# Optimization experiments

Hardware: AMD Instinct MI355X
Metric: run time of the kernel (lower is better)

Reference implementation:

```python
import jax, jax.numpy as jnp
import numpy as np

N, E, IN_DIM, HID, HEADS, N_CLASSES, N_GRAPHS = 50000, 800000, 128, 64, 4, 16, 64
NEG_SLOPE = 0.2


def setup_inputs() -> dict:
    key = jax.random.key(0)
    ks = jax.random.split(key, 12)
    s = 0.1
    return {
        "x": jax.random.normal(ks[0], (N, IN_DIM), jnp.float32),
        "edge_index": jax.random.randint(ks[1], (2, E), 0, N, jnp.int32),
        "batch": jnp.sort(jax.random.randint(ks[2], (N,), 0, N_GRAPHS, jnp.int32)),
        "W1": jax.random.normal(ks[3], (IN_DIM, HEADS * HID), jnp.float32) * s,
        "a_src1": jax.random.normal(ks[4], (HEADS, HID), jnp.float32) * s,
        "a_dst1": jax.random.normal(ks[5], (HEADS, HID), jnp.float32) * s,
        "b1": jnp.zeros((HEADS * HID,), jnp.float32),
        "W2": jax.random.normal(ks[6], (HEADS * HID, HID), jnp.float32) * s,
        "a_src2": jax.random.normal(ks[7], (1, HID), jnp.float32) * s,
        "a_dst2": jax.random.normal(ks[8], (1, HID), jnp.float32) * s,
        "b2": jnp.zeros((HID,), jnp.float32),
        "fcW": jax.random.normal(ks[9], (HID, N_CLASSES), jnp.float32) * s,
        "fcb": jnp.zeros((N_CLASSES,), jnp.float32),
    }


def gat_conv(x, edge_index, W, a_src, a_dst, bias, concat):
    # PyG GATConv (eval mode): add self loops, per-head linear, additive attention,
    # segment softmax over incoming edges of each destination node, scatter-add.
    n = x.shape[0]
    heads, d = a_src.shape
    h = (x @ W).reshape(n, heads, d)                      # [n, H, d]
    asrc = jnp.einsum('nhd,hd->nh', h, a_src)             # [n, H]
    adst = jnp.einsum('nhd,hd->nh', h, a_dst)             # [n, H]
    loops = jnp.arange(n, dtype=edge_index.dtype)
    src = jnp.concatenate([edge_index[0], loops])         # message sources j
    dst = jnp.concatenate([edge_index[1], loops])         # targets i
    e = jax.nn.leaky_relu(asrc[src] + adst[dst], NEG_SLOPE)  # [E+n, H]
    m = jax.ops.segment_max(e, dst, num_segments=n)
    p = jnp.exp(e - m[dst])
    s = jax.ops.segment_sum(p, dst, num_segments=n)
    alpha = p / (s[dst] + 1e-16)                          # [E+n, H]
    msg = h[src] * alpha[:, :, None]                      # [E+n, H, d]
    out = jax.ops.segment_sum(msg, dst, num_segments=n)   # [n, H, d]
    out = out.reshape(n, heads * d) if concat else out.mean(axis=1)
    return out + bias


def reference(x, edge_index, batch, W1, a_src1, a_dst1, b1, W2, a_src2, a_dst2, b2, fcW, fcb):
    h = jax.nn.elu(gat_conv(x, edge_index, W1, a_src1, a_dst1, b1, True))
    h = gat_conv(h, edge_index, W2, a_src2, a_dst2, b2, False)
    # global_mean_pool over graph ids
    cnt = jax.ops.segment_sum(jnp.ones((h.shape[0],), h.dtype), batch, num_segments=N_GRAPHS)
    pooled = jax.ops.segment_sum(h, batch, num_segments=N_GRAPHS) / jnp.maximum(cnt, 1.0)[:, None]
    return pooled @ fcW + fcb
```

## Files before the change

kernel.cpp:

```cpp
#include <hip/hip_runtime.h>
#include <hip/hip_bf16.h>
#include <hip/hip_fp8.h>


#define Nn 50000
#define Ed 800000
#define NEG 0.2f
#define SCAN_B 196
#define EB 3125
#define GB 783

typedef __attribute__((ext_vector_type(8))) short short8;
typedef __attribute__((ext_vector_type(4))) float f32x4;
typedef __attribute__((ext_vector_type(2))) float f32x2;

#if defined(__has_builtin)
#if __has_builtin(__builtin_amdgcn_cvt_pk_f32_fp8) && __has_builtin(__builtin_amdgcn_cvt_pk_fp8_f32)
#define FP8_FAST 1
#endif
#endif
#ifndef FP8_FAST
#define FP8_FAST 0
#endif

__device__ __forceinline__ float lrelu(float x){ return fmaxf(x, NEG*x); }
__device__ __forceinline__ float bf2f(unsigned short u){ return __uint_as_float((unsigned)u << 16); }
__device__ __forceinline__ unsigned short f2bf(float f){
    __hip_bfloat16 b = __float2bfloat16(f);
    return *reinterpret_cast<unsigned short*>(&b);
}
__device__ __forceinline__ short f2bfs(float f){ return (short)f2bf(f); }

__device__ __forceinline__ unsigned char f2fp8(float f){
#if FP8_FAST
    int v = __builtin_amdgcn_cvt_pk_fp8_f32(f, f, 0, false);
    return (unsigned char)(v & 0xff);
#else
    __hip_fp8_e4m3 t(f);
    return (unsigned char)t.__x;
#endif
}

__device__ __forceinline__ float4 fp8x4_to_f32(unsigned int v){
#if FP8_FAST
    f32x2 lo = __builtin_amdgcn_cvt_pk_f32_fp8((int)v, false);
    f32x2 hi = __builtin_amdgcn_cvt_pk_f32_fp8((int)v, true);
    return make_float4(lo[0], lo[1], hi[0], hi[1]);
#else
    __hip_fp8_e4m3 t0, t1, t2, t3;
    t0.__x = (unsigned char)(v);
    t1.__x = (unsigned char)(v >> 8);
    t2.__x = (unsigned char)(v >> 16);
    t3.__x = (unsigned char)(v >> 24);
    return make_float4((float)t0, (float)t1, (float)t2, (float)t3);
#endif
}

__global__ void k_degree(const int* __restrict__ dst, int* __restrict__ deg,
                         const float* __restrict__ W1, const float* __restrict__ W2,
                         unsigned short* __restrict__ W1s, unsigned short* __restrict__ W2s){
    if (blockIdx.x < EB){
        int e = blockIdx.x*256 + threadIdx.x;
        if (e < Ed) atomicAdd(&deg[dst[e]], 1);
    } else {
        int t = (blockIdx.x - EB)*256 + threadIdx.x;
        if (t < 32768){
            int j = t & 7, lane = (t>>3) & 63, ks = (t>>9) & 3, nt = t>>11;
            int k = ks*32 + (lane>>4)*8 + j;
            int n = nt*16 + (lane&15);
            W1s[t] = f2bf(W1[k*256 + n]);
        }
        if (t < 16384){
            int j = t & 7, lane = (t>>3) & 63, ks = (t>>9) & 7, nt = t>>12;
            int k = ks*32 + (lane>>4)*8 + j;
            int n = nt*16 + (lane&15);
            W2s[t] = f2bf(W2[k*64 + n]);
        }
    }
}

__global__ __launch_bounds__(256) void k_partial(const int* __restrict__ deg, int* __restrict__ partial){
    __shared__ int red[256];
    int tid = threadIdx.x;
    int g = blockIdx.x*256 + tid;
    red[tid] = (g < Nn) ? deg[g] : 0;
    __syncthreads();
    for (int off = 128; off > 0; off >>= 1){
        if (tid < off) red[tid] += red[tid+off];
        __syncthreads();
    }
    if (tid == 0) partial[blockIdx.x] = red[0];
}

__global__ __launch_bounds__(256) void k_apply(const int* __restrict__ deg, const int* __restrict__ partial,
                                               int* __restrict__ rowptr, int* __restrict__ cursor){
    __shared__ int sp[256];
    __shared__ int s[256];
    __shared__ int blockoff;
    int tid = threadIdx.x;
    int pv = (tid < SCAN_B) ? partial[tid] : 0;
    sp[tid] = pv; __syncthreads();
    for (int off = 1; off < 256; off <<= 1){
        int t = (tid >= off) ? sp[tid-off] : 0;
        __syncthreads();
        sp[tid] += t;
        __syncthreads();
    }
    if (tid == (int)blockIdx.x) blockoff = sp[tid] - pv;
    if (blockIdx.x == 0 && tid == 255) rowptr[Nn] = sp[255];
    __syncthreads();
    int g = blockIdx.x*256 + tid;
    int v = (g < Nn) ? deg[g] : 0;
    s[tid] = v; __syncthreads();
    for (int off = 1; off < 256; off <<= 1){
        int t = (tid >= off) ? s[tid-off] : 0;
        __syncthreads();
        s[tid] += t;
        __syncthreads();
    }
    if (g < Nn){
        int ex = s[tid] - v + blockoff;
        rowptr[g] = ex;
        cursor[g] = ex;
    }
}

__global__ __launch_bounds__(256) void k_gemm1_scatter(
        const float* __restrict__ x, const unsigned short* __restrict__ W1s,
        const float* __restrict__ a_src, const float* __restrict__ a_dst,
        unsigned char* __restrict__ h1f8,
        float* __restrict__ asrc, float* __restrict__ adst,
        const int* __restrict__ esrc, const int* __restrict__ edst,
        int* __restrict__ cursor, int* __restrict__ csr){
    if (blockIdx.x >= GB){
        int e = (blockIdx.x - GB)*256 + threadIdx.x;
        if (e < Ed){
            int pos = atomicAdd(&cursor[edst[e]], 1);
            csr[pos] = esrc[e];
        }
        return;
    }
    int wv = blockIdx.x*4 + (threadIdx.x>>6);
    int lane = threadIdx.x & 63;
    int m0 = wv*16;
    if (m0 >= Nn) return;
    int quad = lane >> 4, col = lane & 15;
    int mrow = m0 + col;
    f32x4 acc[16] = {};
    const float* ap0 = &x[(size_t)mrow*128 + quad*8];
    #pragma unroll
    for (int ks = 0; ks < 4; ks++){
        float4 a0 = *(const float4*)(ap0 + ks*32);
        float4 a1 = *(const float4*)(ap0 + ks*32 + 4);
        short8 af;
        af[0]=f2bfs(a0.x); af[1]=f2bfs(a0.y); af[2]=f2bfs(a0.z); af[3]=f2bfs(a0.w);
        af[4]=f2bfs(a1.x); af[5]=f2bfs(a1.y); af[6]=f2bfs(a1.z); af[7]=f2bfs(a1.w);
        #pragma unroll
        for (int nt = 0; nt < 16; nt++){
            short8 bf = *(const short8*)&W1s[(size_t)(nt*4+ks)*512 + lane*8];
            acc[nt] = __builtin_amdgcn_mfma_f32_16x16x32_bf16(af, bf, acc[nt], 0, 0, 0);
        }
    }
    unsigned char* outp = &h1f8[(size_t)(m0 + quad*4)*256 + col];
    #pragma unroll
    for (int nt = 0; nt < 16; nt++)
        #pragma unroll
        for (int r = 0; r < 4; r++)
            outp[(size_t)r*256 + nt*16] = f2fp8(acc[nt][r]);
    float asf[16], adf[16];
    #pragma unroll
    for (int nt = 0; nt < 16; nt++){
        asf[nt] = a_src[nt*16 + col];
        adf[nt] = a_dst[nt*16 + col];
    }
    #pragma unroll
    for (int h = 0; h < 4; h++){
        #pragma unroll
        for (int r = 0; r < 4; r++){
            float ps = acc[4*h+0][r]*asf[4*h+0] + acc[4*h+1][r]*asf[4*h+1]
                     + acc[4*h+2][r]*asf[4*h+2] + acc[4*h+3][r]*asf[4*h+3];
            float pd = acc[4*h+0][r]*adf[4*h+0] + acc[4*h+1][r]*adf[4*h+1]
                     + acc[4*h+2][r]*adf[4*h+2] + acc[4*h+3][r]*adf[4*h+3];
            #pragma unroll
            for (int m = 1; m < 16; m <<= 1){ ps += __shfl_xor(ps, m); pd += __shfl_xor(pd, m); }
            if (col == h*4 + r){
                int n = m0 + quad*4 + r;
                asrc[n*4 + h] = ps;
                adst[n*4 + h] = pd;
            }
        }
    }
}

__global__ __launch_bounds__(256) void k_gemm2(const unsigned short* __restrict__ g1b,
                                               const unsigned short* __restrict__ W2s,
                                               const float* __restrict__ a_src, const float* __restrict__ a_dst,
                                               unsigned short* __restrict__ h2b,
                                               float* __restrict__ asrc, float* __restrict__ adst){
    int wv = blockIdx.x*4 + (threadIdx.x>>6);
    int lane = threadIdx.x & 63;
    int m0 = wv*16;
    if (m0 >= Nn) return;
    int quad = lane >> 4, col = lane & 15;
    int mrow = m0 + col;
    f32x4 acc[4] = {};
    const unsigned short* ap0 = &g1b[(size_t)mrow*256 + quad*8];
    #pragma unroll
    for (int ks = 0; ks < 8; ks++){
        short8 af = *(const short8*)(ap0 + ks*32);
        #pragma unroll
        for (int nt = 0; nt < 4; nt++){
            short8 bf = *(const short8*)&W2s[(size_t)(nt*8+ks)*512 + lane*8];
            acc[nt] = __builtin_amdgcn_mfma_f32_16x16x32_bf16(af, bf, acc[nt], 0, 0, 0);
        }
    }
    unsigned short* outp = &h2b[(size_t)(m0 + quad*4)*64 + col];
    #pragma unroll
    for (int nt = 0; nt < 4; nt++)
        #pragma unroll
        for (int r = 0; r < 4; r++)
            outp[(size_t)r*64 + nt*16] = f2bf(acc[nt][r]);
    float asf[4], adf[4];
    #pragma unroll
    for (int nt = 0; nt < 4; nt++){
        asf[nt] = a_src[nt*16 + col];
        adf[nt] = a_dst[nt*16 + col];
    }
    #pragma unroll
    for (int r = 0; r < 4; r++){
        float ps = acc[0][r]*asf[0] + acc[1][r]*asf[1] + acc[2][r]*asf[2] + acc[3][r]*asf[3];
        float pd = acc[0][r]*adf[0] + acc[1][r]*adf[1] + acc[2][r]*adf[2] + acc[3][r]*adf[3];
        #pragma unroll
        for (int m = 1; m < 16; m <<= 1){ ps += __shfl_xor(ps, m); pd += __shfl_xor(pd, m); }
        if (col == r){
            int n = m0 + quad*4 + r;
            asrc[n] = ps;
            adst[n] = pd;
        }
    }
}

__global__ __launch_bounds__(256) void k_aggr1(const unsigned char* __restrict__ h1f8,
                                               const float* __restrict__ asrc, const float* __restrict__ adst,
                                               const int* __restrict__ rowptr, const int* __restrict__ csr,
                                               const float* __restrict__ b1, unsigned short* __restrict__ g1){
    int w = threadIdx.x >> 6, lane = threadIdx.x & 63;
    int i = blockIdx.x*4 + w; if (i >= Nn) return;
    int hh = lane >> 4;
    float ad = adst[i*4 + hh];
    float as = asrc[i*4 + hh];
    float p = __expf(lrelu(as + ad));
    unsigned int hv = *(const unsigned int*)&h1f8[(size_t)i*256 + 4*lane];
    float4 hd = fp8x4_to_f32(hv);
    float acc0 = p*hd.x, acc1 = p*hd.y, acc2 = p*hd.z, acc3 = p*hd.w;
    float ssum = p;
    int beg = rowptr[i], end = rowptr[i+1];
    int j = beg;
    for (; j + 3 < end; j += 4){
        int s0 = csr[j], s1 = csr[j+1], s2 = csr[j+2], s3 = csr[j+3];
        float a0 = asrc[s0*4 + hh];
        float a1 = asrc[s1*4 + hh];
        float a2 = asrc[s2*4 + hh];
        float a3 = asrc[s3*4 + hh];
        unsigned int v0 = *(const unsigned int*)&h1f8[(size_t)s0*256 + 4*lane];
        unsigned int v1 = *(const unsigned int*)&h1f8[(size_t)s1*256 + 4*lane];
        unsigned int v2 = *(const unsigned int*)&h1f8[(size_t)s2*256 + 4*lane];
        unsigned int v3 = *(const unsigned int*)&h1f8[(size_t)s3*256 + 4*lane];
        float q0 = __expf(lrelu(a0 + ad));
        float q1 = __expf(lrelu(a1 + ad));
        float q2 = __expf(lrelu(a2 + ad));
        float q3 = __expf(lrelu(a3 + ad));
        float4 d0 = fp8x4_to_f32(v0);
        float4 d1 = fp8x4_to_f32(v1);
        float4 d2 = fp8x4_to_f32(v2);
        float4 d3 = fp8x4_to_f32(v3);
        acc0 += q0*d0.x + q1*d1.x + q2*d2.x + q3*d3.x;
        acc1 += q0*d0.y + q1*d1.y + q2*d2.y + q3*d3.y;
        acc2 += q0*d0.z + q1*d1.z + q2*d2.z + q3*d3.z;
        acc3 += q0*d0.w + q1*d1.w + q2*d2.w + q3*d3.w;
        ssum += q0 + q1 + q2 + q3;
    }
    for (; j < end; j++){
        int s = csr[j];
        float a = asrc[s*4 + hh];
        unsigned int v = *(const unsigned int*)&h1f8[(size_t)s*256 + 4*lane];
        float q = __expf(lrelu(a + ad));
        float4 d = fp8x4_to_f32(v);
        acc0 += q*d.x; acc1 += q*d.y; acc2 += q*d.z; acc3 += q*d.w;
        ssum += q;
    }
    float inv = 1.0f/(ssum + 1e-16f);
    float4 b4 = *(const float4*)&b1[4*lane];
    float o0 = acc0*inv + b4.x;
    float o1 = acc1*inv + b4.y;
    float o2 = acc2*inv + b4.z;
    float o3 = acc3*inv + b4.w;
    ushort4 o;
    o.x = f2bf(o0 > 0.f ? o0 : expm1f(o0));
    o.y = f2bf(o1 > 0.f ? o1 : expm1f(o1));
    o.z = f2bf(o2 > 0.f ? o2 : expm1f(o2));
    o.w = f2bf(o3 > 0.f ? o3 : expm1f(o3));
    *(ushort4*)&g1[(size_t)i*256 + 4*lane] = o;
}

__global__ __launch_bounds__(256) void k_aggr2(const unsigned short* __restrict__ h2,
                                               const float* __restrict__ asrc, const float* __restrict__ adst,
                                               const int* __restrict__ rowptr, const int* __restrict__ csr,
                                               unsigned short* __restrict__ g2){
    int w = threadIdx.x >> 6, lane = threadIdx.x & 63;
    int i = blockIdx.x*4 + w; if (i >= Nn) return;
    float ad = adst[i];
    float p = __expf(lrelu(asrc[i] + ad));
    float acc = p * bf2f(h2[(size_t)i*64 + lane]);
    float ss = p;
    int beg = rowptr[i], end = rowptr[i+1];
    int j = beg;
    for (; j + 3 < end; j += 4){
        int s0 = csr[j], s1 = csr[j+1], s2 = csr[j+2], s3 = csr[j+3];
        float a0 = asrc[s0], a1 = asrc[s1], a2 = asrc[s2], a3 = asrc[s3];
        unsigned short v0 = h2[(size_t)s0*64 + lane];
        unsigned short v1 = h2[(size_t)s1*64 + lane];
        unsigned short v2 = h2[(size_t)s2*64 + lane];
        unsigned short v3 = h2[(size_t)s3*64 + lane];
        float q0 = __expf(lrelu(a0 + ad));
        float q1 = __expf(lrelu(a1 + ad));
        float q2 = __expf(lrelu(a2 + ad));
        float q3 = __expf(lrelu(a3 + ad));
        acc += q0*bf2f(v0) + q1*bf2f(v1) + q2*bf2f(v2) + q3*bf2f(v3);
        ss += q0 + q1 + q2 + q3;
    }
    for (; j < end; j++){
        int s = csr[j];
        float q = __expf(lrelu(asrc[s] + ad));
        acc += q * bf2f(h2[(size_t)s*64 + lane]);
        ss += q;
    }
    g2[(size_t)i*64 + lane] = f2bf(acc/(ss + 1e-16f));
}

__global__ __launch_bounds__(256) void k_head(const unsigned short* __restrict__ g2,
                                              const int* __restrict__ batch,
                                              const float* __restrict__ b2,
                                              const float* __restrict__ fcW, const float* __restrict__ fcb,
                                              float* __restrict__ out){
    int g = blockIdx.x;
    int w = threadIdx.x >> 6, lane = threadIdx.x & 63;
    int lo = 0, hi = Nn;
    while (lo < hi){ int mid = (lo+hi)>>1; if (batch[mid] < g) lo = mid+1; else hi = mid; }
    int first = lo;
    lo = 0; hi = Nn;
    while (lo < hi){ int mid = (lo+hi)>>1; if (batch[mid] < g+1) lo = mid+1; else hi = mid; }
    int last = lo;
    float acc = 0.f;
    int n = first + w;
    for (; n + 4 < last; n += 8){
        acc += bf2f(g2[(size_t)n*64 + lane]);
        acc += bf2f(g2[(size_t)(n+4)*64 + lane]);
    }
    for (; n < last; n += 4) acc += bf2f(g2[(size_t)n*64 + lane]);
    __shared__ float part[4][64];
    part[w][lane] = acc;
    __syncthreads();
    if (w == 0){
        float tot = part[0][lane] + part[1][lane] + part[2][lane] + part[3][lane];
        float inv = 1.0f / fmaxf((float)(last - first), 1.0f);
        float val = tot*inv + b2[lane];
        #pragma unroll
        for (int c = 0; c < 16; c++){
            float t = val * fcW[lane*16 + c];
            #pragma unroll
            for (int m = 1; m < 64; m <<= 1) t += __shfl_xor(t, m);
            if (lane == 0) out[g*16 + c] = t + fcb[c];
        }
    }
}

extern "C" void kernel_launch(void* const* d_in, const int* in_sizes, int n_in,
                              void* d_out, int out_size, void* d_ws, size_t ws_size,
                              hipStream_t stream) {
    const float* x      = (const float*)d_in[0];
    const int*   ei     = (const int*)d_in[1];
    const int*   batch  = (const int*)d_in[2];
    const float* W1     = (const float*)d_in[3];
    const float* a_src1 = (const float*)d_in[4];
    const float* a_dst1 = (const float*)d_in[5];
    const float* b1     = (const float*)d_in[6];
    const float* W2     = (const float*)d_in[7];
    const float* a_src2 = (const float*)d_in[8];
    const float* a_dst2 = (const float*)d_in[9];
    const float* b2     = (const float*)d_in[10];
    const float* fcW    = (const float*)d_in[11];
    const float* fcb    = (const float*)d_in[12];
    float* out = (float*)d_out;

    char* ws = (char*)d_ws;
    size_t off = 0;
    auto carve = [&](size_t bytes)->void*{
        void* p = ws + off;
        off += (bytes + 255) & ~(size_t)255;
        return p;
    };
    int* deg = (int*)carve((size_t)Nn*4);
    size_t zero_bytes = off;

    unsigned char*  h1f8 = (unsigned char*)carve((size_t)Nn*256);
    unsigned short* g1b  = (unsigned short*)carve((size_t)Nn*256*2);
    unsigned short* h2b  = (unsigned short*)carve((size_t)Nn*64*2);
    unsigned short* g2b  = (unsigned short*)carve((size_t)Nn*64*2);
    float* asrc1  = (float*)carve((size_t)Nn*4*4);
    float* adst1  = (float*)carve((size_t)Nn*4*4);
    float* asrc2  = (float*)carve((size_t)Nn*4);
    float* adst2  = (float*)carve((size_t)Nn*4);
    int*   rowptr = (int*)carve((size_t)(Nn+1)*4);
    int*   cursor = (int*)carve((size_t)Nn*4);
    int*   csr    = (int*)carve((size_t)Ed*4);
    int*   partial= (int*)carve((size_t)SCAN_B*4);
    unsigned short* W1s = (unsigned short*)carve(32768*2);
    unsigned short* W2s = (unsigned short*)carve(16384*2);

    hipMemsetAsync(ws, 0, zero_bytes, stream);

    const int NB4 = (Nn + 3)/4;

    k_degree<<<EB + 128, 256, 0, stream>>>(ei + Ed, deg, W1, W2, W1s, W2s);
    k_partial<<<SCAN_B, 256, 0, stream>>>(deg, partial);
    k_apply<<<SCAN_B, 256, 0, stream>>>(deg, partial, rowptr, cursor);
    k_gemm1_scatter<<<GB + EB, 256, 0, stream>>>(x, W1s, a_src1, a_dst1, h1f8, asrc1, adst1,
                                                 ei, ei + Ed, cursor, csr);
    k_aggr1<<<NB4, 256, 0, stream>>>(h1f8, asrc1, adst1, rowptr, csr, b1, g1b);

    k_gemm2<<<GB, 256, 0, stream>>>(g1b, W2s, a_src2, a_dst2, h2b, asrc2, adst2);
    k_aggr2<<<NB4, 256, 0, stream>>>(h2b, asrc2, adst2, rowptr, csr, g2b);

    k_head<<<64, 256, 0, stream>>>(g2b, batch, b2, fcW, fcb, out);
}
```

Before: 326.4 us.

## Fuse CSR build stages into one cooperative kernel with grid syncs

Replaces the memset, degree count, two scan kernels and the edge scatter with a single cooperative kernel. It uses grid-wide syncs between zeroing, degree counting, partial reduction, scan and scatter, which removes several launches and the memset. The CSR scatter is no longer overlapped with the GEMM1 blocks, so gemm1 now runs alone afterward. The grid syncs add their own cost, and the fixed 1024-block grid must fit co-resident for the cooperative launch to work.

```diff
diff --git a/kernel.cpp b/kernel.cpp
--- a/kernel.cpp
+++ b/kernel.cpp
@@ -1,14 +1,17 @@
 #include <hip/hip_runtime.h>
 #include <hip/hip_bf16.h>
 #include <hip/hip_fp8.h>
+#include <hip/hip_cooperative_groups.h>
 
 
 #define Nn 50000
 #define Ed 800000
 #define NEG 0.2f
 #define SCAN_B 196
-#define EB 3125
+#define CSR_BLOCKS 1024
 #define GB 783
+
+namespace cg = cooperative_groups;
 
 typedef __attribute__((ext_vector_type(8))) short short8;
 typedef __attribute__((ext_vector_type(4))) float f32x4;
@@ -56,90 +59,92 @@
 #endif
 }
 
-__global__ void k_degree(const int* __restrict__ dst, int* __restrict__ deg,
-                         const float* __restrict__ W1, const float* __restrict__ W2,
-                         unsigned short* __restrict__ W1s, unsigned short* __restrict__ W2s){
-    if (blockIdx.x < EB){
-        int e = blockIdx.x*256 + threadIdx.x;
-        if (e < Ed) atomicAdd(&deg[dst[e]], 1);
-    } else {
-        int t = (blockIdx.x - EB)*256 + threadIdx.x;
-        if (t < 32768){
-            int j = t & 7, lane = (t>>3) & 63, ks = (t>>9) & 3, nt = t>>11;
-            int k = ks*32 + (lane>>4)*8 + j;
-            int n = nt*16 + (lane&15);
-            W1s[t] = f2bf(W1[k*256 + n]);
-        }
-        if (t < 16384){
-            int j = t & 7, lane = (t>>3) & 63, ks = (t>>9) & 7, nt = t>>12;
-            int k = ks*32 + (lane>>4)*8 + j;
-            int n = nt*16 + (lane&15);
-            W2s[t] = f2bf(W2[k*64 + n]);
-        }
-    }
-}
-
-__global__ __launch_bounds__(256) void k_partial(const int* __restrict__ deg, int* __restrict__ partial){
-    __shared__ int red[256];
-    int tid = threadIdx.x;
-    int g = blockIdx.x*256 + tid;
-    red[tid] = (g < Nn) ? deg[g] : 0;
-    __syncthreads();
-    for (int off = 128; off > 0; off >>= 1){
-        if (tid < off) red[tid] += red[tid+off];
+__global__ __launch_bounds__(256) void k_csr(const int* __restrict__ esrc, const int* __restrict__ edst,
+                                             const float* __restrict__ W1, const float* __restrict__ W2,
+                                             unsigned short* __restrict__ W1s, unsigned short* __restrict__ W2s,
+                                             int* __restrict__ deg, int* __restrict__ partial,
+                                             int* __restrict__ rowptr, int* __restrict__ cursor,
+                                             int* __restrict__ csr){
+    cg::grid_group grid = cg::this_grid();
+    const int tid = threadIdx.x;
+    const int b = blockIdx.x;
+    const int gstride = CSR_BLOCKS*256;
+    const int gt = b*256 + tid;
+
+    for (int i = gt; i < Nn; i += gstride) deg[i] = 0;
+    for (int t = gt; t < 32768; t += gstride){
+        int j = t & 7, lane = (t>>3) & 63, ks = (t>>9) & 3, nt = t>>11;
+        W1s[t] = f2bf(W1[(ks*32 + (lane>>4)*8 + j)*256 + nt*16 + (lane&15)]);
+    }
+    for (int t = gt; t < 16384; t += gstride){
+        int j = t & 7, lane = (t>>3) & 63, ks = (t>>9) & 7, nt = t>>12;
+        W2s[t] = f2bf(W2[(ks*32 + (lane>>4)*8 + j)*64 + nt*16 + (lane&15)]);
+    }
+    __threadfence();
+    grid.sync();
+
+    for (int e = gt; e < Ed; e += gstride) atomicAdd(&deg[edst[e]], 1);
+    __threadfence();
+    grid.sync();
+
+    if (b < SCAN_B){
+        __shared__ int red[256];
+        int g = b*256 + tid;
+        red[tid] = (g < Nn) ? deg[g] : 0;
         __syncthreads();
-    }
-    if (tid == 0) partial[blockIdx.x] = red[0];
-}
-
-__global__ __launch_bounds__(256) void k_apply(const int* __restrict__ deg, const int* __restrict__ partial,
-                                               int* __restrict__ rowptr, int* __restrict__ cursor){
-    __shared__ int sp[256];
-    __shared__ int s[256];
-    __shared__ int blockoff;
-    int tid = threadIdx.x;
-    int pv = (tid < SCAN_B) ? partial[tid] : 0;
-    sp[tid] = pv; __syncthreads();
-    for (int off = 1; off < 256; off <<= 1){
-        int t = (tid >= off) ? sp[tid-off] : 0;
+        for (int off = 128; off > 0; off >>= 1){
+            if (tid < off) red[tid] += red[tid+off];
+            __syncthreads();
+        }
+        if (tid == 0) partial[b] = red[0];
+    }
+    __threadfence();
+    grid.sync();
+
+    if (b < SCAN_B){
+        __shared__ int sp[256];
+        __shared__ int s[256];
+        __shared__ int blockoff;
+        int pv = (tid < SCAN_B) ? partial[tid] : 0;
+        sp[tid] = pv; __syncthreads();
+        for (int off = 1; off < 256; off <<= 1){
+            int t = (tid >= off) ? sp[tid-off] : 0;
+            __syncthreads();
+            sp[tid] += t;
+            __syncthreads();
+        }
+        if (tid == b) blockoff = sp[tid] - pv;
+        if (b == 0 && tid == 255) rowptr[Nn] = sp[255];
         __syncthreads();
-        sp[tid] += t;
-        __syncthreads();
-    }
-    if (tid == (int)blockIdx.x) blockoff = sp[tid] - pv;
-    if (blockIdx.x == 0 && tid == 255) rowptr[Nn] = sp[255];
-    __syncthreads();
-    int g = blockIdx.x*256 + tid;
-    int v = (g < Nn) ? deg[g] : 0;
-    s[tid] = v; __syncthreads();
-    for (int off = 1; off < 256; off <<= 1){
-        int t = (tid >= off) ? s[tid-off] : 0;
-        __syncthreads();
-        s[tid] += t;
-        __syncthreads();
-    }
-    if (g < Nn){
-        int ex = s[tid] - v + blockoff;
-        rowptr[g] = ex;
-        cursor[g] = ex;
-    }
-}
-
-__global__ __launch_bounds__(256) void k_gemm1_scatter(
-        const float* __restrict__ x, const unsigned short* __restrict__ W1s,
-        const float* __restrict__ a_src, const float* __restrict__ a_dst,
-        unsigned char* __restrict__ h1f8,
-        float* __restrict__ asrc, float* __restrict__ adst,
-        const int* __restrict__ esrc, const int* __restrict__ edst,
-        int* __restrict__ cursor, int* __restrict__ csr){
-    if (blockIdx.x >= GB){
-        int e = (blockIdx.x - GB)*256 + threadIdx.x;
-        if (e < Ed){
-            int pos = atomicAdd(&cursor[edst[e]], 1);
-            csr[pos] = esrc[e];
-        }
-        return;
-    }
+        int g = b*256 + tid;
+        int v = (g < Nn) ? deg[g] : 0;
+        s[tid] = v; __syncthreads();
+        for (int off = 1; off < 256; off <<= 1){
+            int t = (tid >= off) ? s[tid-off] : 0;
+            __syncthreads();
+            s[tid] += t;
+            __syncthreads();
+        }
+        if (g < Nn){
+            int ex = s[tid] - v + blockoff;
+            rowptr[g] = ex;
+            cursor[g] = ex;
+        }
+    }
+    __threadfence();
+    grid.sync();
+
+    for (int e = gt; e < Ed; e += gstride){
+        int pos = atomicAdd(&cursor[edst[e]], 1);
+        csr[pos] = esrc[e];
+    }
+}
+
+__global__ __launch_bounds__(256) void k_gemm1(const float* __restrict__ x,
+                                               const unsigned short* __restrict__ W1s,
+                                               const float* __restrict__ a_src, const float* __restrict__ a_dst,
+                                               unsigned char* __restrict__ h1f8,
+                                               float* __restrict__ asrc, float* __restrict__ adst){
     int wv = blockIdx.x*4 + (threadIdx.x>>6);
     int lane = threadIdx.x & 63;
     int m0 = wv*16;
@@ -401,7 +406,6 @@
         return p;
     };
     int* deg = (int*)carve((size_t)Nn*4);
-    size_t zero_bytes = off;
 
     unsigned char*  h1f8 = (unsigned char*)carve((size_t)Nn*256);
     unsigned short* g1b  = (unsigned short*)carve((size_t)Nn*256*2);
@@ -418,15 +422,18 @@
     unsigned short* W1s = (unsigned short*)carve(32768*2);
     unsigned short* W2s = (unsigned short*)carve(16384*2);
 
-    hipMemsetAsync(ws, 0, zero_bytes, stream);
-
     const int NB4 = (Nn + 3)/4;
 
-    k_degree<<<EB + 128, 256, 0, stream>>>(ei + Ed, deg, W1, W2, W1s, W2s);
-    k_partial<<<SCAN_B, 256, 0, stream>>>(deg, partial);
-    k_apply<<<SCAN_B, 256, 0, stream>>>(deg, partial, rowptr, cursor);
-    k_gemm1_scatter<<<GB + EB, 256, 0, stream>>>(x, W1s, a_src1, a_dst1, h1f8, asrc1, adst1,
-                                                 ei, ei + Ed, cursor, csr);
+    const int* esrc = ei;
+    const int* edst = ei + Ed;
+    void* csr_args[] = {
+        (void*)&esrc, (void*)&edst,
+        (void*)&W1, (void*)&W2, (void*)&W1s, (void*)&W2s,
+        (void*)&deg, (void*)&partial, (void*)&rowptr, (void*)&cursor, (void*)&csr
+    };
+    hipLaunchCooperativeKernel((void*)k_csr, dim3(CSR_BLOCKS), dim3(256), csr_args, 0, stream);
+
+    k_gemm1<<<GB, 256, 0, stream>>>(x, W1s, a_src1, a_dst1, h1f8, asrc1, adst1);
     k_aggr1<<<NB4, 256, 0, stream>>>(h1f8, asrc1, adst1, rowptr, csr, b1, g1b);
 
     k_gemm2<<<GB, 256, 0, stream>>>(g1b, W2s, a_src2, a_dst2, h2b, asrc2, adst2);
```

New measurement: 955.1 us. 2.93x slower.

## Fuse layer-1 aggregation with layer-2 GEMM and merge scan kernels

Applied to the files above, without the earlier changes.

The layer-1 aggregation now stages each block's four output rows in shared memory, and one wave runs the bf16 MFMA projection to layer 2 plus the attention logits. This removes the global round-trip of the 50000x256 bf16 intermediate and one kernel launch. The price is that each 16-row MFMA tile now has only 4 valid rows, so three quarters of the matrix work is wasted, and the other three waves sit idle during the GEMM. Separately, the two-kernel prefix scan becomes one kernel in which each block re-sums all preceding degrees to get its offset, which adds redundant reads.

```diff
diff --git a/kernel.cpp b/kernel.cpp
--- a/kernel.cpp
+++ b/kernel.cpp
@@ -9,6 +9,7 @@
 #define SCAN_B 196
 #define EB 3125
 #define GB 783
+#define NB4 12500
 
 typedef __attribute__((ext_vector_type(8))) short short8;
 typedef __attribute__((ext_vector_type(4))) float f32x4;
@@ -66,49 +67,29 @@
         int t = (blockIdx.x - EB)*256 + threadIdx.x;
         if (t < 32768){
             int j = t & 7, lane = (t>>3) & 63, ks = (t>>9) & 3, nt = t>>11;
-            int k = ks*32 + (lane>>4)*8 + j;
-            int n = nt*16 + (lane&15);
-            W1s[t] = f2bf(W1[k*256 + n]);
+            W1s[t] = f2bf(W1[(ks*32 + (lane>>4)*8 + j)*256 + nt*16 + (lane&15)]);
         }
         if (t < 16384){
             int j = t & 7, lane = (t>>3) & 63, ks = (t>>9) & 7, nt = t>>12;
-            int k = ks*32 + (lane>>4)*8 + j;
-            int n = nt*16 + (lane&15);
-            W2s[t] = f2bf(W2[k*64 + n]);
-        }
-    }
-}
-
-__global__ __launch_bounds__(256) void k_partial(const int* __restrict__ deg, int* __restrict__ partial){
+            W2s[t] = f2bf(W2[(ks*32 + (lane>>4)*8 + j)*64 + nt*16 + (lane&15)]);
+        }
+    }
+}
+
+__global__ __launch_bounds__(256) void k_apply(const int* __restrict__ deg,
+                                               int* __restrict__ rowptr, int* __restrict__ cursor){
     __shared__ int red[256];
+    __shared__ int s[256];
     int tid = threadIdx.x;
-    int g = blockIdx.x*256 + tid;
-    red[tid] = (g < Nn) ? deg[g] : 0;
-    __syncthreads();
+    int lim = blockIdx.x*256;
+    int part = 0;
+    for (int i = tid; i < lim; i += 256) part += deg[i];
+    red[tid] = part; __syncthreads();
     for (int off = 128; off > 0; off >>= 1){
         if (tid < off) red[tid] += red[tid+off];
         __syncthreads();
     }
-    if (tid == 0) partial[blockIdx.x] = red[0];
-}
-
-__global__ __launch_bounds__(256) void k_apply(const int* __restrict__ deg, const int* __restrict__ partial,
-                                               int* __restrict__ rowptr, int* __restrict__ cursor){
-    __shared__ int sp[256];
-    __shared__ int s[256];
-    __shared__ int blockoff;
-    int tid = threadIdx.x;
-    int pv = (tid < SCAN_B) ? partial[tid] : 0;
-    sp[tid] = pv; __syncthreads();
-    for (int off = 1; off < 256; off <<= 1){
-        int t = (tid >= off) ? sp[tid-off] : 0;
-        __syncthreads();
-        sp[tid] += t;
-        __syncthreads();
-    }
-    if (tid == (int)blockIdx.x) blockoff = sp[tid] - pv;
-    if (blockIdx.x == 0 && tid == 255) rowptr[Nn] = sp[255];
-    __syncthreads();
+    int blockoff = red[0];
     int g = blockIdx.x*256 + tid;
     int v = (g < Nn) ? deg[g] : 0;
     s[tid] = v; __syncthreads();
@@ -123,6 +104,7 @@
         rowptr[g] = ex;
         cursor[g] = ex;
     }
+    if (blockIdx.x == SCAN_B-1 && tid == 255) rowptr[Nn] = blockoff + s[255];
 }
 
 __global__ __launch_bounds__(256) void k_gemm1_scatter(
@@ -192,60 +174,18 @@
     }
 }
 
-__global__ __launch_bounds__(256) void k_gemm2(const unsigned short* __restrict__ g1b,
-                                               const unsigned short* __restrict__ W2s,
-                                               const float* __restrict__ a_src, const float* __restrict__ a_dst,
-                                               unsigned short* __restrict__ h2b,
-                                               float* __restrict__ asrc, float* __restrict__ adst){
-    int wv = blockIdx.x*4 + (threadIdx.x>>6);
-    int lane = threadIdx.x & 63;
-    int m0 = wv*16;
-    if (m0 >= Nn) return;
-    int quad = lane >> 4, col = lane & 15;
-    int mrow = m0 + col;
-    f32x4 acc[4] = {};
-    const unsigned short* ap0 = &g1b[(size_t)mrow*256 + quad*8];
-    #pragma unroll
-    for (int ks = 0; ks < 8; ks++){
-        short8 af = *(const short8*)(ap0 + ks*32);
-        #pragma unroll
-        for (int nt = 0; nt < 4; nt++){
-            short8 bf = *(const short8*)&W2s[(size_t)(nt*8+ks)*512 + lane*8];
-            acc[nt] = __builtin_amdgcn_mfma_f32_16x16x32_bf16(af, bf, acc[nt], 0, 0, 0);
-        }
-    }
-    unsigned short* outp = &h2b[(size_t)(m0 + quad*4)*64 + col];
-    #pragma unroll
-    for (int nt = 0; nt < 4; nt++)
-        #pragma unroll
-        for (int r = 0; r < 4; r++)
-            outp[(size_t)r*64 + nt*16] = f2bf(acc[nt][r]);
-    float asf[4], adf[4];
-    #pragma unroll
-    for (int nt = 0; nt < 4; nt++){
-        asf[nt] = a_src[nt*16 + col];
-        adf[nt] = a_dst[nt*16 + col];
-    }
-    #pragma unroll
-    for (int r = 0; r < 4; r++){
-        float ps = acc[0][r]*asf[0] + acc[1][r]*asf[1] + acc[2][r]*asf[2] + acc[3][r]*asf[3];
-        float pd = acc[0][r]*adf[0] + acc[1][r]*adf[1] + acc[2][r]*adf[2] + acc[3][r]*adf[3];
-        #pragma unroll
-        for (int m = 1; m < 16; m <<= 1){ ps += __shfl_xor(ps, m); pd += __shfl_xor(pd, m); }
-        if (col == r){
-            int n = m0 + quad*4 + r;
-            asrc[n] = ps;
-            adst[n] = pd;
-        }
-    }
-}
-
-__global__ __launch_bounds__(256) void k_aggr1(const unsigned char* __restrict__ h1f8,
-                                               const float* __restrict__ asrc, const float* __restrict__ adst,
-                                               const int* __restrict__ rowptr, const int* __restrict__ csr,
-                                               const float* __restrict__ b1, unsigned short* __restrict__ g1){
+__global__ __launch_bounds__(256) void k_aggr1_gemm2(
+        const unsigned char* __restrict__ h1f8,
+        const float* __restrict__ asrc, const float* __restrict__ adst,
+        const int* __restrict__ rowptr, const int* __restrict__ csr,
+        const float* __restrict__ b1,
+        const unsigned short* __restrict__ W2s,
+        const float* __restrict__ a_src2, const float* __restrict__ a_dst2,
+        unsigned short* __restrict__ h2b,
+        float* __restrict__ asrc2, float* __restrict__ adst2){
+    __shared__ unsigned short g1s[4][256];
     int w = threadIdx.x >> 6, lane = threadIdx.x & 63;
-    int i = blockIdx.x*4 + w; if (i >= Nn) return;
+    int i = blockIdx.x*4 + w;
     int hh = lane >> 4;
     float ad = adst[i*4 + hh];
     float as = asrc[i*4 + hh];
@@ -300,7 +240,48 @@
     o.y = f2bf(o1 > 0.f ? o1 : expm1f(o1));
     o.z = f2bf(o2 > 0.f ? o2 : expm1f(o2));
     o.w = f2bf(o3 > 0.f ? o3 : expm1f(o3));
-    *(ushort4*)&g1[(size_t)i*256 + 4*lane] = o;
+    *(ushort4*)&g1s[w][4*lane] = o;
+    __syncthreads();
+
+    if (threadIdx.x >= 64) return;
+    int quad = lane >> 4, col = lane & 15;
+    int m = col;
+    int m0 = blockIdx.x*4;
+    f32x4 acc2g[4] = {};
+    #pragma unroll
+    for (int ks = 0; ks < 8; ks++){
+        short8 af = {0,0,0,0,0,0,0,0};
+        if (m < 4) af = *(const short8*)&g1s[m][ks*32 + quad*8];
+        #pragma unroll
+        for (int nt = 0; nt < 4; nt++){
+            short8 bf = *(const short8*)&W2s[(size_t)(nt*8+ks)*512 + lane*8];
+            acc2g[nt] = __builtin_amdgcn_mfma_f32_16x16x32_bf16(af, bf, acc2g[nt], 0, 0, 0);
+        }
+    }
+    if (quad == 0){
+        #pragma unroll
+        for (int nt = 0; nt < 4; nt++)
+            #pragma unroll
+            for (int r = 0; r < 4; r++)
+                h2b[(size_t)(m0 + r)*64 + nt*16 + col] = f2bf(acc2g[nt][r]);
+    }
+    float asf[4], adf[4];
+    #pragma unroll
+    for (int nt = 0; nt < 4; nt++){
+        asf[nt] = a_src2[nt*16 + col];
+        adf[nt] = a_dst2[nt*16 + col];
+    }
+    #pragma unroll
+    for (int r = 0; r < 4; r++){
+        float ps = acc2g[0][r]*asf[0] + acc2g[1][r]*asf[1] + acc2g[2][r]*asf[2] + acc2g[3][r]*asf[3];
+        float pd = acc2g[0][r]*adf[0] + acc2g[1][r]*adf[1] + acc2g[2][r]*adf[2] + acc2g[3][r]*adf[3];
+        #pragma unroll
+        for (int mm = 1; mm < 16; mm <<= 1){ ps += __shfl_xor(ps, mm); pd += __shfl_xor(pd, mm); }
+        if (quad == 0 && col == r){
+            asrc2[m0 + r] = ps;
+            adst2[m0 + r] = pd;
+        }
+    }
 }
 
 __global__ __launch_bounds__(256) void k_aggr2(const unsigned short* __restrict__ h2,
@@ -404,7 +385,6 @@
     size_t zero_bytes = off;
 
     unsigned char*  h1f8 = (unsigned char*)carve((size_t)Nn*256);
-    unsigned short* g1b  = (unsigned short*)carve((size_t)Nn*256*2);
     unsigned short* h2b  = (unsigned short*)carve((size_t)Nn*64*2);
     unsigned short* g2b  = (unsigned short*)carve((size_t)Nn*64*2);
     float* asrc1  = (float*)carve((size_t)Nn*4*4);
@@ -414,23 +394,17 @@
     int*   rowptr = (int*)carve((size_t)(Nn+1)*4);
     int*   cursor = (int*)carve((size_t)Nn*4);
     int*   csr    = (int*)carve((size_t)Ed*4);
-    int*   partial= (int*)carve((size_t)SCAN_B*4);
     unsigned short* W1s = (unsigned short*)carve(32768*2);
     unsigned short* W2s = (unsigned short*)carve(16384*2);
 
     hipMemsetAsync(ws, 0, zero_bytes, stream);
 
-    const int NB4 = (Nn + 3)/4;
-
     k_degree<<<EB + 128, 256, 0, stream>>>(ei + Ed, deg, W1, W2, W1s, W2s);
-    k_partial<<<SCAN_B, 256, 0, stream>>>(deg, partial);
-    k_apply<<<SCAN_B, 256, 0, stream>>>(deg, partial, rowptr, cursor);
+    k_apply<<<SCAN_B, 256, 0, stream>>>(deg, rowptr, cursor);
     k_gemm1_scatter<<<GB + EB, 256, 0, stream>>>(x, W1s, a_src1, a_dst1, h1f8, asrc1, adst1,
                                                  ei, ei + Ed, cursor, csr);
-    k_aggr1<<<NB4, 256, 0, stream>>>(h1f8, asrc1, adst1, rowptr, csr, b1, g1b);
-
-    k_gemm2<<<GB, 256, 0, stream>>>(g1b, W2s, a_src2, a_dst2, h2b, asrc2, adst2);
+    k_aggr1_gemm2<<<NB4, 256, 0, stream>>>(h1f8, asrc1, adst1, rowptr, csr, b1,
+                                           W2s, a_src2, a_dst2, h2b, asrc2, adst2);
     k_aggr2<<<NB4, 256, 0, stream>>>(h2b, asrc2, adst2, rowptr, csr, g2b);
-
     k_head<<<64, 256, 0, stream>>>(g2b, batch, b2, fcW, fcb, out);
 }
```

Measured after the change: 363.2 us. +11.3%, slower.
